# Optimization experiments

Measured on AMD Instinct MI355X. Metric: run time of the kernel, lower is better.

## Reference

```python
import jax, jax.numpy as jnp
import numpy as np

B, T, C = 8, 1024, 1024
H, HS = 16, 64            # n_head, head_size
K, STRIDE = 32, 16        # block_length, stride_length
WIN = 128                 # local_window_size
EPS = 1e-5


def _ln(z, w):
    m = jnp.mean(z, axis=-1, keepdims=True)
    v = jnp.var(z, axis=-1, keepdims=True)
    return (z - m) / jnp.sqrt(v + EPS) * w


def setup_inputs() -> dict:
    key = jax.random.key(0)
    ks = jax.random.split(key, 8)
    s = 0.02
    return {
        "x": jax.random.normal(ks[0], (B, T, C), jnp.float32),
        "c_attn_w": jax.random.normal(ks[1], (3 * C, C), jnp.float32) * s,
        "conv_w": jax.random.normal(ks[2], (HS, HS, K), jnp.float32) * s,
        "ln_comp_w": jnp.ones((HS,), jnp.float32),
        "ln_local_w": jnp.ones((C,), jnp.float32),
        "gate_w1": jax.random.normal(ks[3], (C, 2 * C), jnp.float32) * s,
        "gate_ln_w": jnp.ones((C,), jnp.float32),
        "gate_w2": jax.random.normal(ks[4], (2, C), jnp.float32) * s,
        "c_proj_w": jax.random.normal(ks[5], (C, C), jnp.float32) * s,
    }


def reference(x, c_attn_w, conv_w, ln_comp_w, ln_local_w, gate_w1, gate_ln_w, gate_w2, c_proj_w):
    qkv = jnp.einsum('btc,oc->bto', x, c_attn_w)          # [B,T,3C]
    q, k, v = jnp.split(qkv, 3, axis=-1)
    def heads(t):
        return t.reshape(B, T, H, HS).transpose(0, 2, 1, 3)  # [B,H,T,hs]
    q, k, v = heads(q), heads(k), heads(v)

    # CompressionMLP: Conv1d over time + LayerNorm(hs) + exact GELU
    def compress(t):
        xr = t.transpose(0, 1, 3, 2).reshape(B * H, HS, T)   # [B*H, hs, T]
        co = jax.lax.conv_general_dilated(
            xr, conv_w, window_strides=(STRIDE,), padding='VALID',
            dimension_numbers=('NCH', 'OIH', 'NCH'))          # [B*H, hs, NB]
        co = co.transpose(0, 2, 1)                            # [B*H, NB, hs]
        co = jax.nn.gelu(_ln(co, ln_comp_w), approximate=False)
        nb = co.shape[1]
        return co.reshape(B, H, nb, HS)

    kc = compress(k)
    vc = compress(v)
    NB = kc.shape[2]  # 63
    scale = 1.0 / np.sqrt(HS)

    ti = jnp.arange(T)
    band = (ti[None, :] <= ti[:, None]) & (ti[None, :] >= ti[:, None] - WIN)  # [T,T]
    s_loc = jnp.einsum('bhqd,bhkd->bhqk', q, k) * scale
    s_loc = jnp.where(band[None, None], s_loc, -jnp.inf)
    local_out = jnp.einsum('bhqk,bhkd->bhqd', jax.nn.softmax(s_loc, axis=-1), v)
    local_out = local_out.transpose(0, 2, 1, 3).reshape(B, T, C)
    local_norm = _ln(local_out, ln_local_w)

    # compressed-KV attention with block-causal mask: block j <= token i
    bj = jnp.arange(NB)
    cmask = bj[None, :] <= ti[:, None]                        # [T,NB]
    s_cmp = jnp.einsum('bhqd,bhkd->bhqk', q, kc) * scale
    s_cmp = jnp.where(cmask[None, None], s_cmp, -jnp.inf)
    comp_out = jnp.einsum('bhqk,bhkd->bhqd', jax.nn.softmax(s_cmp, axis=-1), vc)
    comp_out = comp_out.transpose(0, 2, 1, 3).reshape(B, T, C)

    # AttentionGating: last-token features -> Linear -> LN -> ReLU -> Linear -> softmax
    feats = jnp.concatenate([local_norm[:, -1, :], comp_out[:, -1, :]], axis=-1)  # [B,2C]
    h = jax.nn.relu(_ln(feats @ gate_w1.T, gate_ln_w))
    gates = jax.nn.softmax(h @ gate_w2.T, axis=-1)            # [B,2]

    combined = gates[:, None, 0:1] * local_norm + gates[:, None, 1:2] * comp_out
    y = jnp.einsum('btc,oc->bto', combined, c_proj_w)
    return y
```

## Files before the change

### kernel.cpp

```cpp
#include <hip/hip_runtime.h>
#include <cstdint>
#include <cmath>
#include <cstddef>

typedef unsigned int u32;
typedef unsigned short u16;
typedef __bf16 bf16x8 __attribute__((ext_vector_type(8)));
typedef float f32x4 __attribute__((ext_vector_type(4)));
typedef u32 u32x4 __attribute__((ext_vector_type(4)));
typedef u32 u32x2 __attribute__((ext_vector_type(2)));

#define DEV static __device__ __forceinline__

DEV float bflo(u32 u) { return __uint_as_float(u << 16); }
DEV float bfhi(u32 u) { return __uint_as_float(u & 0xffff0000u); }
DEV u16 f2bf(float f) {
  u32 u = __float_as_uint(f);
  u += 0x7fffu + ((u >> 16) & 1u);
  return (u16)(u >> 16);
}
DEV f32x4 unpack_bf4(u32x2 r) {
  return (f32x4){bflo(r[0]), bfhi(r[0]), bflo(r[1]), bfhi(r[1])};
}
DEV float wredsum(float v) {
#pragma unroll
  for (int o = 32; o; o >>= 1) v += __shfl_xor(v, o, 64);
  return v;
}

DEV void gload_lds16(const u16* g, u16* lds_base) {
  __builtin_amdgcn_global_load_lds((const __attribute__((address_space(1))) void*)g,
                                   (__attribute__((address_space(3))) void*)lds_base,
                                   16, 0, 0);
}

__global__ __launch_bounds__(256) void fused_cast(const float* __restrict__ x,
                                                  const float* __restrict__ aw,
                                                  const float* __restrict__ pw,
                                                  const float* __restrict__ cw,
                                                  u16* __restrict__ xb,
                                                  u16* __restrict__ wab,
                                                  u16* __restrict__ wpb,
                                                  u16* __restrict__ wcb,
                                                  u16* __restrict__ kcb,
                                                  u16* __restrict__ vcb) {
  const int blk = blockIdx.x;
  if (blk < 12288) {
    const float* src;
    u16* dst;
    int base;
    if (blk < 8192) { src = x; dst = xb; base = blk; }
    else if (blk < 11264) { src = aw; dst = wab; base = blk - 8192; }
    else { src = pw; dst = wpb; base = blk - 11264; }
    const size_t idx = ((size_t)base * 256 + threadIdx.x) * 4;
    const f32x4 v = *(const f32x4*)&src[idx];
    u32x2 r;
    r[0] = (u32)f2bf(v[0]) | ((u32)f2bf(v[1]) << 16);
    r[1] = (u32)f2bf(v[2]) | ((u32)f2bf(v[3]) << 16);
    *(u32x2*)&dst[idx] = r;
  } else if (blk < 12800) {
    const int idx = (blk - 12288) * 256 + threadIdx.x;
    const int o = idx >> 11;
    const int rest = idx & 2047;
    const int i = rest >> 5;
    const int kk = rest & 31;
    wcb[(o << 11) + (kk << 6) + i] = f2bf(cw[idx]);
  } else {
    for (int i = threadIdx.x; i < 8192; i += 256) {
      const int bh = i >> 6, d = i & 63;
      kcb[bh * 4096 + 63 * 64 + d] = 0;
      vcb[bh * 4096 + d * 64 + 63] = 0;
    }
  }
}

template <int OUT_BF16>
__global__ __launch_bounds__(256) void gemm_bt(const u16* __restrict__ A,
                                               const u16* __restrict__ Bm,
                                               void* __restrict__ out,
                                               int M, int N, int K) {
  __shared__ u16 As[128 * 32];
  __shared__ u16 Bs[128 * 32];
  const int tid = threadIdx.x;
  const int lane = tid & 63;
  const int w = tid >> 6;
  const int row0 = blockIdx.x * 128;
  const int col0 = blockIdx.y * 128;
  const int wm = (w >> 1) * 64, wn = (w & 1) * 64;
  const int lr = lane & 15, lq = lane >> 4;
  const int srow = lane >> 2;
  const int scol = (lane & 3) * 8;

  f32x4 acc[4][4] = {};

  for (int k0 = 0; k0 < K; k0 += 32) {
    __syncthreads();
#pragma unroll
    for (int p = 0; p < 2; ++p) {
      const int base_r = p * 64 + w * 16;
      gload_lds16(&A[(size_t)(row0 + base_r + srow) * K + k0 + scol], &As[base_r * 32]);
      gload_lds16(&Bm[(size_t)(col0 + base_r + srow) * K + k0 + scol], &Bs[base_r * 32]);
    }
    __syncthreads();
    bf16x8 af[4], bfr[4];
#pragma unroll
    for (int i = 0; i < 4; ++i) {
      af[i] = *(const bf16x8*)&As[(wm + i * 16 + lr) * 32 + lq * 8];
      bfr[i] = *(const bf16x8*)&Bs[(wn + i * 16 + lr) * 32 + lq * 8];
    }
#pragma unroll
    for (int i = 0; i < 4; ++i)
#pragma unroll
      for (int j = 0; j < 4; ++j)
        acc[i][j] = __builtin_amdgcn_mfma_f32_16x16x32_bf16(af[i], bfr[j], acc[i][j], 0, 0, 0);
  }
#pragma unroll
  for (int i = 0; i < 4; ++i)
#pragma unroll
    for (int j = 0; j < 4; ++j)
#pragma unroll
      for (int rr = 0; rr < 4; ++rr) {
        const int gr = row0 + wm + i * 16 + lq * 4 + rr;
        const int gc = col0 + wn + j * 16 + lr;
        const float v = acc[i][j][rr];
        if (OUT_BF16)
          ((u16*)out)[(size_t)gr * N + gc] = f2bf(v);
        else
          ((float*)out)[(size_t)gr * N + gc] = v;
      }
}

__global__ __launch_bounds__(256) void compress_kernel(const u16* __restrict__ qkv,
                                                       const u16* __restrict__ Wc,
                                                       const float* __restrict__ ln_w,
                                                       u16* __restrict__ kcb,
                                                       u16* __restrict__ vcb) {
  __shared__ u16 As[128 * 32];
  __shared__ u16 Bs[64 * 32];
  __shared__ float Cs[128][65];
  const int srcoff = 1024 + (int)blockIdx.y * 1024;
  const int tid = threadIdx.x;
  const int lane = tid & 63;
  const int w = tid >> 6;
  const int r0 = blockIdx.x * 128;
  const int lr = lane & 15, lq = lane >> 4;

  size_t rowbase[2];
#pragma unroll
  for (int p = 0; p < 2; ++p) {
    const int idx = p * 256 + tid;
    const int r = idx >> 2, c = (idx & 3) * 8;
    const int gr = r0 + r;
    const int bh = gr / 63;
    const int nb = gr - bh * 63;
    const int b = bh >> 4, h = bh & 15;
    rowbase[p] = (size_t)(b * 1024 + nb * 16) * 3072 + srcoff + h * 64 + c;
  }
  const int brow = tid >> 2, bcol = (tid & 3) * 8;

  f32x4 acc[2][4] = {};
  for (int k0 = 0; k0 < 2048; k0 += 32) {
    const int kk = k0 >> 6;
    const int i0 = k0 & 63;
    __syncthreads();
#pragma unroll
    for (int p = 0; p < 2; ++p) {
      const int idx = p * 256 + tid;
      const int r = idx >> 2, c = (idx & 3) * 8;
      *(u32x4*)&As[r * 32 + c] = *(const u32x4*)&qkv[rowbase[p] + (size_t)kk * 3072 + i0];
    }
    *(u32x4*)&Bs[brow * 32 + bcol] = *(const u32x4*)&Wc[(size_t)brow * 2048 + k0 + bcol];
    __syncthreads();
    bf16x8 af[2], bfr[4];
#pragma unroll
    for (int i = 0; i < 2; ++i) af[i] = *(const bf16x8*)&As[(w * 32 + i * 16 + lr) * 32 + lq * 8];
#pragma unroll
    for (int j = 0; j < 4; ++j) bfr[j] = *(const bf16x8*)&Bs[(j * 16 + lr) * 32 + lq * 8];
#pragma unroll
    for (int i = 0; i < 2; ++i)
#pragma unroll
      for (int j = 0; j < 4; ++j)
        acc[i][j] = __builtin_amdgcn_mfma_f32_16x16x32_bf16(af[i], bfr[j], acc[i][j], 0, 0, 0);
  }
  __syncthreads();
#pragma unroll
  for (int i = 0; i < 2; ++i)
#pragma unroll
    for (int j = 0; j < 4; ++j)
#pragma unroll
      for (int rr = 0; rr < 4; ++rr)
        Cs[w * 32 + i * 16 + lq * 4 + rr][j * 16 + lr] = acc[i][j][rr];
  __syncthreads();
  if (tid < 128) {
    const int r = tid;
    const int gr = r0 + r;
    const int bh2 = gr / 63;
    const int nb2 = gr - bh2 * 63;
    float s = 0.f, s2 = 0.f;
#pragma unroll 8
    for (int d = 0; d < 64; ++d) {
      const float xv = Cs[r][d];
      s += xv;
      s2 += xv * xv;
    }
    const float m = s * (1.f / 64.f);
    const float inv = rsqrtf(s2 * (1.f / 64.f) - m * m + 1e-5f);
    if (blockIdx.y == 0) {
      const size_t gb = (size_t)bh2 * 4096 + nb2 * 64;
#pragma unroll 8
      for (int d = 0; d < 64; ++d) {
        const float z = (Cs[r][d] - m) * inv * ln_w[d];
        kcb[gb + d] = f2bf(0.5f * z * (1.f + erff(z * 0.70710678118f)));
      }
    } else {
      const size_t gb = (size_t)bh2 * 4096 + nb2;
#pragma unroll 8
      for (int d = 0; d < 64; ++d) {
        const float z = (Cs[r][d] - m) * inv * ln_w[d];
        vcb[gb + d * 64] = f2bf(0.5f * z * (1.f + erff(z * 0.70710678118f)));
      }
    }
  }
}

__global__ __launch_bounds__(256) void attn_fused(const u16* __restrict__ qkv,
                                                  const u16* __restrict__ kcb,
                                                  const u16* __restrict__ vcb,
                                                  u16* __restrict__ loc,
                                                  u16* __restrict__ outc) {
  __shared__ __align__(16) char smem[53248];
  u16* Ks = (u16*)smem;
  u16* Vt = (u16*)smem;
  u16* Ps = (u16*)(smem + 27648);
  const int bh = blockIdx.x;
  const int b = bh >> 4, h = bh & 15;
  const int i0 = blockIdx.y * 64;
  const int jbase = i0 - 128;
  const int tid = threadIdx.x;
  const int lane = tid & 63, w = tid >> 6;
  const int lr = lane & 15, lq = lane >> 4;

  u32x4 vreg[6];
#pragma unroll
  for (int c = 0; c < 6; ++c) {
    const int lin = c * 256 + tid;
    const int s = lin >> 3, d0 = (lin & 7) * 8;
    const int j = jbase + s;
    u32x4 kval = {0, 0, 0, 0}, vval = {0, 0, 0, 0};
    if (j >= 0) {
      const size_t ro = (size_t)(b * 1024 + j) * 3072 + h * 64 + d0;
      kval = *(const u32x4*)&qkv[ro + 1024];
      vval = *(const u32x4*)&qkv[ro + 2048];
    }
    vreg[c] = vval;
    *(u32x4*)&Ks[s * 72 + d0] = kval;
  }
  bf16x8 qf[2];
  {
    const size_t qrow = (size_t)(b * 1024 + i0 + w * 16 + lr) * 3072 + h * 64;
#pragma unroll
    for (int ks = 0; ks < 2; ++ks) qf[ks] = *(const bf16x8*)&qkv[qrow + ks * 32 + lq * 8];
  }
  __syncthreads();

  f32x4 sa[9];
#pragma unroll
  for (int j9 = 0; j9 < 9; ++j9) sa[j9] = (f32x4){0.f, 0.f, 0.f, 0.f};
#pragma unroll
  for (int ks = 0; ks < 2; ++ks)
#pragma unroll
    for (int j9 = 0; j9 < 9; ++j9) {
      const int jt = w + j9;
      const bf16x8 kf = *(const bf16x8*)&Ks[(jt * 16 + lr) * 72 + ks * 32 + lq * 8];
      sa[j9] = __builtin_amdgcn_mfma_f32_16x16x32_bf16(qf[ks], kf, sa[j9], 0, 0, 0);
    }

  const float NINF = -__builtin_inff();
  float mx[4] = {NINF, NINF, NINF, NINF};
#pragma unroll
  for (int j9 = 0; j9 < 9; ++j9) {
    const int s = (w + j9) * 16 + lr;
#pragma unroll
    for (int rr = 0; rr < 4; ++rr) {
      const int qi = w * 16 + lq * 4 + rr;
      const bool valid = (jbase + s >= 0) && (s >= qi) && (s <= qi + 128);
      const float v = valid ? sa[j9][rr] * 0.125f : NINF;
      sa[j9][rr] = v;
      mx[rr] = fmaxf(mx[rr], v);
    }
  }
#pragma unroll
  for (int rr = 0; rr < 4; ++rr)
#pragma unroll
    for (int o = 1; o < 16; o <<= 1) mx[rr] = fmaxf(mx[rr], __shfl_xor(mx[rr], o, 64));
  float sum[4] = {0.f, 0.f, 0.f, 0.f};
#pragma unroll
  for (int j9 = 0; j9 < 9; ++j9)
#pragma unroll
    for (int rr = 0; rr < 4; ++rr) {
      const float p = __expf(sa[j9][rr] - mx[rr]);
      sa[j9][rr] = p;
      sum[rr] += p;
    }
#pragma unroll
  for (int rr = 0; rr < 4; ++rr) {
#pragma unroll
    for (int o = 1; o < 16; o <<= 1) sum[rr] += __shfl_xor(sum[rr], o, 64);
    sum[rr] = 1.0f / sum[rr];
  }
  __syncthreads();

#pragma unroll
  for (int j9 = 0; j9 < 9; ++j9) {
    const int jt = w + j9;
#pragma unroll
    for (int rr = 0; rr < 4; ++rr)
      Ps[(w * 16 + lq * 4 + rr) * 200 + jt * 16 + lr] = f2bf(sa[j9][rr] * sum[rr]);
  }
  {
    const int jz = (w == 0) ? 9 : (w == 1) ? 0 : (w == 2) ? 11 : 2;
#pragma unroll
    for (int rr = 0; rr < 4; ++rr) Ps[(w * 16 + lq * 4 + rr) * 200 + jz * 16 + lr] = 0;
  }
#pragma unroll
  for (int c = 0; c < 6; ++c) {
    const int lin = c * 256 + tid;
    const int s = lin >> 3, d0 = (lin & 7) * 8;
    const u32x4 val = vreg[c];
#pragma unroll
    for (int q = 0; q < 4; ++q) {
      Vt[(d0 + 2 * q) * 200 + s] = (u16)(val[q] & 0xffffu);
      Vt[(d0 + 2 * q + 1) * 200 + s] = (u16)(val[q] >> 16);
    }
  }
  __syncthreads();

  const int W = (w >> 1) * 32;
  f32x4 oa[4];
#pragma unroll
  for (int jt = 0; jt < 4; ++jt) oa[jt] = (f32x4){0.f, 0.f, 0.f, 0.f};
#pragma unroll
  for (int ks = 0; ks < 5; ++ks) {
    const bf16x8 pf = *(const bf16x8*)&Ps[(w * 16 + lr) * 200 + W + ks * 32 + lq * 8];
#pragma unroll
    for (int jt = 0; jt < 4; ++jt) {
      const bf16x8 vf = *(const bf16x8*)&Vt[(jt * 16 + lr) * 200 + W + ks * 32 + lq * 8];
      oa[jt] = __builtin_amdgcn_mfma_f32_16x16x32_bf16(pf, vf, oa[jt], 0, 0, 0);
    }
  }
#pragma unroll
  for (int jt = 0; jt < 4; ++jt)
#pragma unroll
    for (int rr = 0; rr < 4; ++rr)
      loc[(size_t)(b * 1024 + i0 + w * 16 + lq * 4 + rr) * 1024 + h * 64 + jt * 16 + lr] =
          f2bf(oa[jt][rr]);

  __syncthreads();
  u16* Kc = (u16*)smem;
  u16* Vc = (u16*)(smem + 9216);
  u16* Pc = (u16*)(smem + 18432);
  const size_t cb = (size_t)bh * 4096;
  for (int c2 = tid; c2 < 512; c2 += 256) {
    const int nb = c2 >> 3, d0 = (c2 & 7) * 8;
    *(u32x4*)&Kc[nb * 72 + d0] = *(const u32x4*)&kcb[cb + nb * 64 + d0];
  }
  for (int c2 = tid; c2 < 512; c2 += 256) {
    const int d = c2 >> 3, n0 = (c2 & 7) * 8;
    *(u32x4*)&Vc[d * 72 + n0] = *(const u32x4*)&vcb[cb + d * 64 + n0];
  }
  __syncthreads();

  f32x4 ca[4];
#pragma unroll
  for (int j = 0; j < 4; ++j) ca[j] = (f32x4){0.f, 0.f, 0.f, 0.f};
#pragma unroll
  for (int ks = 0; ks < 2; ++ks)
#pragma unroll
    for (int j = 0; j < 4; ++j) {
      const bf16x8 kf = *(const bf16x8*)&Kc[(j * 16 + lr) * 72 + ks * 32 + lq * 8];
      ca[j] = __builtin_amdgcn_mfma_f32_16x16x32_bf16(qf[ks], kf, ca[j], 0, 0, 0);
    }
  float mc[4] = {NINF, NINF, NINF, NINF};
#pragma unroll
  for (int j = 0; j < 4; ++j) {
    const int s = j * 16 + lr;
#pragma unroll
    for (int rr = 0; rr < 4; ++rr) {
      const int i = i0 + w * 16 + lq * 4 + rr;
      const bool valid = (s <= i) && (s < 63);
      const float v = valid ? ca[j][rr] * 0.125f : NINF;
      ca[j][rr] = v;
      mc[rr] = fmaxf(mc[rr], v);
    }
  }
#pragma unroll
  for (int rr = 0; rr < 4; ++rr)
#pragma unroll
    for (int o = 1; o < 16; o <<= 1) mc[rr] = fmaxf(mc[rr], __shfl_xor(mc[rr], o, 64));
  float sc[4] = {0.f, 0.f, 0.f, 0.f};
#pragma unroll
  for (int j = 0; j < 4; ++j)
#pragma unroll
    for (int rr = 0; rr < 4; ++rr) {
      const float p = __expf(ca[j][rr] - mc[rr]);
      ca[j][rr] = p;
      sc[rr] += p;
    }
#pragma unroll
  for (int rr = 0; rr < 4; ++rr) {
#pragma unroll
    for (int o = 1; o < 16; o <<= 1) sc[rr] += __shfl_xor(sc[rr], o, 64);
    sc[rr] = 1.0f / sc[rr];
  }
#pragma unroll
  for (int j = 0; j < 4; ++j)
#pragma unroll
    for (int rr = 0; rr < 4; ++rr)
      Pc[(w * 16 + lq * 4 + rr) * 72 + j * 16 + lr] = f2bf(ca[j][rr] * sc[rr]);
  __syncthreads();

  f32x4 co[4];
#pragma unroll
  for (int jt = 0; jt < 4; ++jt) co[jt] = (f32x4){0.f, 0.f, 0.f, 0.f};
#pragma unroll
  for (int ks = 0; ks < 2; ++ks) {
    const bf16x8 pf = *(const bf16x8*)&Pc[(w * 16 + lr) * 72 + ks * 32 + lq * 8];
#pragma unroll
    for (int jt = 0; jt < 4; ++jt) {
      const bf16x8 vf = *(const bf16x8*)&Vc[(jt * 16 + lr) * 72 + ks * 32 + lq * 8];
      co[jt] = __builtin_amdgcn_mfma_f32_16x16x32_bf16(pf, vf, co[jt], 0, 0, 0);
    }
  }
#pragma unroll
  for (int jt = 0; jt < 4; ++jt)
#pragma unroll
    for (int rr = 0; rr < 4; ++rr)
      outc[(size_t)(b * 1024 + i0 + w * 16 + lq * 4 + rr) * 1024 + h * 64 + jt * 16 + lr] =
          f2bf(co[jt][rr]);
}

__global__ __launch_bounds__(256) void ln_feats(const u16* __restrict__ locb,
                                                const u16* __restrict__ compb,
                                                const float* __restrict__ lnw,
                                                float* __restrict__ feats) {
  const int b = blockIdx.x, tid = threadIdx.x;
  const size_t base = ((size_t)b * 1024 + 1023) * 1024 + tid * 4;
  const f32x4 v = unpack_bf4(*(const u32x2*)&locb[base]);
  float s = v[0] + v[1] + v[2] + v[3];
  float s2 = v[0] * v[0] + v[1] * v[1] + v[2] * v[2] + v[3] * v[3];
  s = wredsum(s);
  s2 = wredsum(s2);
  __shared__ float rs[4], rs2[4];
  const int w = tid >> 6, lane = tid & 63;
  if (!lane) { rs[w] = s; rs2[w] = s2; }
  __syncthreads();
  s = rs[0] + rs[1] + rs[2] + rs[3];
  s2 = rs2[0] + rs2[1] + rs2[2] + rs2[3];
  const float m = s * (1.f / 1024.f);
  const float inv = rsqrtf(s2 * (1.f / 1024.f) - m * m + 1e-5f);
  const f32x4 wv = *(const f32x4*)&lnw[tid * 4];
  f32x4 o;
#pragma unroll
  for (int k = 0; k < 4; ++k) o[k] = (v[k] - m) * inv * wv[k];
  *(f32x4*)&feats[b * 2048 + tid * 4] = o;
  *(f32x4*)&feats[b * 2048 + 1024 + tid * 4] = unpack_bf4(*(const u32x2*)&compb[base]);
}

__global__ __launch_bounds__(256) void gate_gemv(const float* __restrict__ feats,
                                                 const float* __restrict__ w1,
                                                 float* __restrict__ hraw) {
  const int o = blockIdx.x * 4 + (threadIdx.x >> 6);
  const int lane = threadIdx.x & 63;
  const float* wr = &w1[(size_t)o * 2048];
  float acc[8] = {};
#pragma unroll
  for (int it = 0; it < 8; ++it) {
    const int c = (it * 64 + lane) * 4;
    const f32x4 wv = *(const f32x4*)&wr[c];
#pragma unroll
    for (int b = 0; b < 8; ++b) {
      const f32x4 fv = *(const f32x4*)&feats[b * 2048 + c];
      acc[b] += fv[0] * wv[0] + fv[1] * wv[1] + fv[2] * wv[2] + fv[3] * wv[3];
    }
  }
#pragma unroll
  for (int b = 0; b < 8; ++b) acc[b] = wredsum(acc[b]);
  if (lane == 0) {
#pragma unroll
    for (int b = 0; b < 8; ++b) hraw[b * 1024 + o] = acc[b];
  }
}

__global__ __launch_bounds__(256) void gate_fin(const float* __restrict__ hraw,
                                                const float* __restrict__ lnw,
                                                const float* __restrict__ w2,
                                                float* __restrict__ gates) {
  const int b = blockIdx.x, tid = threadIdx.x;
  const f32x4 v = *(const f32x4*)&hraw[(size_t)b * 1024 + tid * 4];
  float s = v[0] + v[1] + v[2] + v[3];
  float s2 = v[0] * v[0] + v[1] * v[1] + v[2] * v[2] + v[3] * v[3];
  s = wredsum(s);
  s2 = wredsum(s2);
  __shared__ float rs[4], rs2[4];
  const int w = tid >> 6, lane = tid & 63;
  if (!lane) { rs[w] = s; rs2[w] = s2; }
  __syncthreads();
  s = rs[0] + rs[1] + rs[2] + rs[3];
  s2 = rs2[0] + rs2[1] + rs2[2] + rs2[3];
  const float m = s * (1.f / 1024.f);
  const float inv = rsqrtf(s2 * (1.f / 1024.f) - m * m + 1e-5f);
  float p0 = 0.f, p1 = 0.f;
#pragma unroll
  for (int k = 0; k < 4; ++k) {
    float hh = (v[k] - m) * inv * lnw[tid * 4 + k];
    hh = fmaxf(hh, 0.f);
    p0 += hh * w2[tid * 4 + k];
    p1 += hh * w2[1024 + tid * 4 + k];
  }
  p0 = wredsum(p0);
  p1 = wredsum(p1);
  __syncthreads();
  if (!lane) { rs[w] = p0; rs2[w] = p1; }
  __syncthreads();
  if (tid == 0) {
    const float l0 = rs[0] + rs[1] + rs[2] + rs[3];
    const float l1 = rs2[0] + rs2[1] + rs2[2] + rs2[3];
    const float mm = fmaxf(l0, l1);
    const float e0 = __expf(l0 - mm), e1 = __expf(l1 - mm);
    const float iv = 1.f / (e0 + e1);
    gates[b * 2] = e0 * iv;
    gates[b * 2 + 1] = e1 * iv;
  }
}

__global__ __launch_bounds__(256) void combine_ln_cast(const u16* __restrict__ locb,
                                                       const u16* __restrict__ compb,
                                                       const float* __restrict__ lnw,
                                                       const float* __restrict__ gates,
                                                       u16* __restrict__ outb) {
  const int row = blockIdx.x, tid = threadIdx.x;
  const size_t base = (size_t)row * 1024 + tid * 4;
  const f32x4 v = unpack_bf4(*(const u32x2*)&locb[base]);
  float s = v[0] + v[1] + v[2] + v[3];
  float s2 = v[0] * v[0] + v[1] * v[1] + v[2] * v[2] + v[3] * v[3];
  s = wredsum(s);
  s2 = wredsum(s2);
  __shared__ float rs[4], rs2[4];
  const int w = tid >> 6, lane = tid & 63;
  if (!lane) { rs[w] = s; rs2[w] = s2; }
  __syncthreads();
  s = rs[0] + rs[1] + rs[2] + rs[3];
  s2 = rs2[0] + rs2[1] + rs2[2] + rs2[3];
  const float m = s * (1.f / 1024.f);
  const float inv = rsqrtf(s2 * (1.f / 1024.f) - m * m + 1e-5f);
  const int b = row >> 10;
  const float g0 = gates[2 * b], g1 = gates[2 * b + 1];
  const f32x4 wv = *(const f32x4*)&lnw[tid * 4];
  const f32x4 c = unpack_bf4(*(const u32x2*)&compb[base]);
  float ov[4];
#pragma unroll
  for (int k = 0; k < 4; ++k) ov[k] = g0 * ((v[k] - m) * inv * wv[k]) + g1 * c[k];
  u32x2 r;
  r[0] = (u32)f2bf(ov[0]) | ((u32)f2bf(ov[1]) << 16);
  r[1] = (u32)f2bf(ov[2]) | ((u32)f2bf(ov[3]) << 16);
  *(u32x2*)&outb[base] = r;
}

extern "C" void kernel_launch(void* const* d_in, const int* in_sizes, int n_in,
                              void* d_out, int out_size, void* d_ws, size_t ws_size,
                              hipStream_t stream) {
  const float* x = (const float*)d_in[0];
  const float* c_attn_w = (const float*)d_in[1];
  const float* conv_w = (const float*)d_in[2];
  const float* ln_comp_w = (const float*)d_in[3];
  const float* ln_local_w = (const float*)d_in[4];
  const float* gate_w1 = (const float*)d_in[5];
  const float* gate_ln_w = (const float*)d_in[6];
  const float* gate_w2 = (const float*)d_in[7];
  const float* c_proj_w = (const float*)d_in[8];
  float* y = (float*)d_out;

  char* ws = (char*)d_ws;
  size_t off = 0;
  auto alloc = [&](size_t bytes) -> void* {
    void* p = ws + off;
    off += (bytes + 255) & ~(size_t)255;
    return p;
  };
  u16* qkvb = (u16*)alloc((size_t)8192 * 3072 * 2);
  u16* xb = (u16*)alloc((size_t)8192 * 1024 * 2);
  u16* wab = (u16*)alloc((size_t)3072 * 1024 * 2);
  u16* wpb = (u16*)alloc((size_t)1024 * 1024 * 2);
  u16* wcb = (u16*)alloc((size_t)64 * 2048 * 2);
  u16* kcb = (u16*)alloc((size_t)128 * 4096 * 2);
  u16* vcb = (u16*)alloc((size_t)128 * 4096 * 2);
  u16* locb = (u16*)alloc((size_t)8192 * 1024 * 2);
  u16* compb = (u16*)alloc((size_t)8192 * 1024 * 2);
  float* feats = (float*)alloc((size_t)8 * 2048 * 4);
  float* hraw = (float*)alloc((size_t)8192 * 4);
  float* gates = (float*)alloc(64);
  u16* combb = (u16*)alloc((size_t)8192 * 1024 * 2);

  fused_cast<<<12801, 256, 0, stream>>>(x, c_attn_w, c_proj_w, conv_w, xb, wab, wpb, wcb, kcb,
                                        vcb);

  gemm_bt<1><<<dim3(64, 24), 256, 0, stream>>>(xb, wab, qkvb, 8192, 3072, 1024);

  compress_kernel<<<dim3(63, 2), 256, 0, stream>>>(qkvb, wcb, ln_comp_w, kcb, vcb);

  attn_fused<<<dim3(128, 16), 256, 0, stream>>>(qkvb, kcb, vcb, locb, compb);

  ln_feats<<<8, 256, 0, stream>>>(locb, compb, ln_local_w, feats);
  gate_gemv<<<256, 256, 0, stream>>>(feats, gate_w1, hraw);
  gate_fin<<<8, 256, 0, stream>>>(hraw, gate_ln_w, gate_w2, gates);

  combine_ln_cast<<<8192, 256, 0, stream>>>(locb, compb, ln_local_w, gates, combb);

  gemm_bt<0><<<dim3(64, 8), 256, 0, stream>>>(combb, wpb, y, 8192, 1024, 1024);
}
```

Baseline: 314.0 us.

## Double-buffer compress GEMM with async LDS loads and halve its tile rows

The compress kernel now uses 64-row tiles with double-buffered shared memory filled by direct global-to-LDS loads, so the next K-slice is prefetched while MFMAs run on the current one. The grid doubles to 126x2 blocks to put more blocks on the machine. The projection GEMM also gets a min-blocks-per-CU launch bound of 4. Risks are extra register pressure in the GEMM, and a dependence on gload_lds16 existing and ordering correctly with the single barrier per iteration.

```diff
diff --git a/kernel.cpp b/kernel.cpp
--- a/kernel.cpp
+++ b/kernel.cpp
@@ -75,10 +75,10 @@
 }
 
 template <int OUT_BF16>
-__global__ __launch_bounds__(256) void gemm_bt(const u16* __restrict__ A,
-                                               const u16* __restrict__ Bm,
-                                               void* __restrict__ out,
-                                               int M, int N, int K) {
+__global__ __launch_bounds__(256, 4) void gemm_bt(const u16* __restrict__ A,
+                                                  const u16* __restrict__ Bm,
+                                                  void* __restrict__ out,
+                                                  int M, int N, int K) {
   __shared__ u16 As[128 * 32];
   __shared__ u16 Bs[128 * 32];
   const int tid = threadIdx.x;
@@ -135,71 +135,59 @@
                                                        const float* __restrict__ ln_w,
                                                        u16* __restrict__ kcb,
                                                        u16* __restrict__ vcb) {
-  __shared__ u16 As[128 * 32];
-  __shared__ u16 Bs[64 * 32];
-  __shared__ float Cs[128][65];
+  __shared__ u16 As[2][64 * 32];
+  __shared__ u16 Bs[2][64 * 32];
+  __shared__ float Cs[64][65];
+  const int tid = threadIdx.x;
+  const int lane = tid & 63, w = tid >> 6;
+  const int lr = lane & 15, lq = lane >> 4;
+  const int r0 = blockIdx.x * 64;
   const int srcoff = 1024 + (int)blockIdx.y * 1024;
-  const int tid = threadIdx.x;
-  const int lane = tid & 63;
-  const int w = tid >> 6;
-  const int r0 = blockIdx.x * 128;
-  const int lr = lane & 15, lq = lane >> 4;
-
-  size_t rowbase[2];
-#pragma unroll
-  for (int p = 0; p < 2; ++p) {
-    const int idx = p * 256 + tid;
-    const int r = idx >> 2, c = (idx & 3) * 8;
-    const int gr = r0 + r;
-    const int bh = gr / 63;
-    const int nb = gr - bh * 63;
-    const int b = bh >> 4, h = bh & 15;
-    rowbase[p] = (size_t)(b * 1024 + nb * 16) * 3072 + srcoff + h * 64 + c;
-  }
-  const int brow = tid >> 2, bcol = (tid & 3) * 8;
-
-  f32x4 acc[2][4] = {};
-  for (int k0 = 0; k0 < 2048; k0 += 32) {
-    const int kk = k0 >> 6;
-    const int i0 = k0 & 63;
+
+  const int arow = tid >> 2, acol = (tid & 3) * 8;
+  const int gr = r0 + arow;
+  const int bh = gr / 63;
+  const int nb = gr - bh * 63;
+  const int b = bh >> 4, h = bh & 15;
+  const size_t abase = (size_t)(b * 1024 + nb * 16) * 3072 + srcoff + h * 64 + acol;
+  const size_t bbase = (size_t)arow * 2048 + acol;
+
+  f32x4 acc[4] = {};
+  {
+    gload_lds16(&qkv[abase], &As[0][w * 512]);
+    gload_lds16(&Wc[bbase], &Bs[0][w * 512]);
+  }
+  for (int it = 0; it < 64; ++it) {
+    const int cur = it & 1;
     __syncthreads();
-#pragma unroll
-    for (int p = 0; p < 2; ++p) {
-      const int idx = p * 256 + tid;
-      const int r = idx >> 2, c = (idx & 3) * 8;
-      *(u32x4*)&As[r * 32 + c] = *(const u32x4*)&qkv[rowbase[p] + (size_t)kk * 3072 + i0];
-    }
-    *(u32x4*)&Bs[brow * 32 + bcol] = *(const u32x4*)&Wc[(size_t)brow * 2048 + k0 + bcol];
-    __syncthreads();
-    bf16x8 af[2], bfr[4];
-#pragma unroll
-    for (int i = 0; i < 2; ++i) af[i] = *(const bf16x8*)&As[(w * 32 + i * 16 + lr) * 32 + lq * 8];
-#pragma unroll
-    for (int j = 0; j < 4; ++j) bfr[j] = *(const bf16x8*)&Bs[(j * 16 + lr) * 32 + lq * 8];
-#pragma unroll
-    for (int i = 0; i < 2; ++i)
-#pragma unroll
-      for (int j = 0; j < 4; ++j)
-        acc[i][j] = __builtin_amdgcn_mfma_f32_16x16x32_bf16(af[i], bfr[j], acc[i][j], 0, 0, 0);
-  }
-  __syncthreads();
-#pragma unroll
-  for (int i = 0; i < 2; ++i)
-#pragma unroll
-    for (int j = 0; j < 4; ++j)
-#pragma unroll
-      for (int rr = 0; rr < 4; ++rr)
-        Cs[w * 32 + i * 16 + lq * 4 + rr][j * 16 + lr] = acc[i][j][rr];
-  __syncthreads();
-  if (tid < 128) {
-    const int r = tid;
-    const int gr = r0 + r;
-    const int bh2 = gr / 63;
-    const int nb2 = gr - bh2 * 63;
+    if (it < 63) {
+      const int k0 = (it + 1) * 32;
+      const int kk = k0 >> 6, i0 = k0 & 63;
+      gload_lds16(&qkv[abase + (size_t)kk * 3072 + i0], &As[cur ^ 1][w * 512]);
+      gload_lds16(&Wc[bbase + k0], &Bs[cur ^ 1][w * 512]);
+    }
+    const bf16x8 af = *(const bf16x8*)&As[cur][(w * 16 + lr) * 32 + lq * 8];
+#pragma unroll
+    for (int j = 0; j < 4; ++j) {
+      const bf16x8 bfr = *(const bf16x8*)&Bs[cur][(j * 16 + lr) * 32 + lq * 8];
+      acc[j] = __builtin_amdgcn_mfma_f32_16x16x32_bf16(af, bfr, acc[j], 0, 0, 0);
+    }
+  }
+  __syncthreads();
+#pragma unroll
+  for (int j = 0; j < 4; ++j)
+#pragma unroll
+    for (int rr = 0; rr < 4; ++rr)
+      Cs[w * 16 + lq * 4 + rr][j * 16 + lr] = acc[j][rr];
+  __syncthreads();
+  if (tid < 64) {
+    const int gr2 = r0 + tid;
+    const int bh2 = gr2 / 63;
+    const int nb2 = gr2 - bh2 * 63;
     float s = 0.f, s2 = 0.f;
 #pragma unroll 8
     for (int d = 0; d < 64; ++d) {
-      const float xv = Cs[r][d];
+      const float xv = Cs[tid][d];
       s += xv;
       s2 += xv * xv;
     }
@@ -209,14 +197,14 @@
       const size_t gb = (size_t)bh2 * 4096 + nb2 * 64;
 #pragma unroll 8
       for (int d = 0; d < 64; ++d) {
-        const float z = (Cs[r][d] - m) * inv * ln_w[d];
+        const float z = (Cs[tid][d] - m) * inv * ln_w[d];
         kcb[gb + d] = f2bf(0.5f * z * (1.f + erff(z * 0.70710678118f)));
       }
     } else {
       const size_t gb = (size_t)bh2 * 4096 + nb2;
 #pragma unroll 8
       for (int d = 0; d < 64; ++d) {
-        const float z = (Cs[r][d] - m) * inv * ln_w[d];
+        const float z = (Cs[tid][d] - m) * inv * ln_w[d];
         vcb[gb + d * 64] = f2bf(0.5f * z * (1.f + erff(z * 0.70710678118f)));
       }
     }
@@ -606,7 +594,7 @@
 
   gemm_bt<1><<<dim3(64, 24), 256, 0, stream>>>(xb, wab, qkvb, 8192, 3072, 1024);
 
-  compress_kernel<<<dim3(63, 2), 256, 0, stream>>>(qkvb, wcb, ln_comp_w, kcb, vcb);
+  compress_kernel<<<dim3(126, 2), 256, 0, stream>>>(qkvb, wcb, ln_comp_w, kcb, vcb);
 
   attn_fused<<<dim3(128, 16), 256, 0, stream>>>(qkvb, kcb, vcb, locb, compb);
 
```

Result: faster. 300.1 us (-4.4%).
